# Kernel tuning notes

Hardware: AMD Instinct MI355X
Metric: run time of the kernel (lower is better)

## Reference

```python
import jax
import jax.numpy as jnp
import numpy as np

KSIZE, STRIDE, RATE, FUSE_K, SCALE = 3, 1, 2, 3, 10.0
ESCAPE_NAN = 1e-4


def _same_pad(x, k, s):
    # replicates torch same_padding: asymmetric zero pad so out = ceil(H/s)
    H, W = x.shape[2], x.shape[3]
    oh, ow = -(-H // s), -(-W // s)
    ph = max(0, (oh - 1) * s + k - H)
    pw = max(0, (ow - 1) * s + k - W)
    return jnp.pad(x, ((0, 0), (0, 0), (ph // 2, ph - ph // 2), (pw // 2, pw - pw // 2)))


def _extract_patches(x, k, s):
    # torch extract_image_patches: -> [B, L, C, k, k] with L = out_h*out_w
    x = _same_pad(x, k, s)
    B, C, H, W = x.shape
    Ho, Wo = (H - k) // s + 1, (W - k) // s + 1
    slices = [x[:, :, i:i + Ho * s:s, j:j + Wo * s:s] for i in range(k) for j in range(k)]
    p = jnp.stack(slices, axis=2).reshape(B, C, k, k, Ho, Wo)
    return p.transpose(0, 4, 5, 1, 2, 3).reshape(B, Ho * Wo, C, k, k)


def _contextual_attention(f, b, mask):
    dn = ('NCHW', 'OIHW', 'NCHW')
    # raw background patches for the final deconv: k = 2*rate, stride = rate
    raw_pat = _extract_patches(b, 2 * RATE, RATE * STRIDE)  # [B, L, C, 4, 4]
    # nearest-neighbor 1/rate downsample (torch F.interpolate nearest, sf=0.5)
    f_ds = f[:, :, ::RATE, ::RATE]
    b_ds = b[:, :, ::RATE, ::RATE]
    m_ds = mask[:, :, ::RATE, ::RATE]
    B, C, Hf, Wf = f_ds.shape
    Hb, Wb = b_ds.shape[2], b_ds.shape[3]
    b_pat = _extract_patches(b_ds, KSIZE, STRIDE)  # [B, L, C, 3, 3], L = Hb*Wb
    m_pat = _extract_patches(m_ds, KSIZE, STRIDE)[0]  # [L, 1, 3, 3] (first sample only, as in torch)
    mm = (jnp.mean(m_pat, axis=(1, 2, 3)) == 0.0).astype(f.dtype)[None, :, None, None]  # [1, L, 1, 1]
    fuse_w = jnp.eye(FUSE_K, dtype=f.dtype).reshape(1, 1, FUSE_K, FUSE_K)

    def per_item(xi, wi, raw_wi):
        # xi: [C,Hf,Wf]; wi: [L,C,3,3]; raw_wi: [L,C,4,4]
        max_wi = jnp.sqrt(jnp.sum(wi * wi + ESCAPE_NAN, axis=(1, 2, 3), keepdims=True))
        wi_n = wi / max_wi
        # matching conv: scores [1, L, Hf, Wf]
        yi = jax.lax.conv_general_dilated(xi[None], wi_n, (1, 1), ((1, 1), (1, 1)), dimension_numbers=dn)
        # fuse: identity-diagonal 3x3 conv along (bg_idx, fg_idx) twice with transposes
        yi = yi.reshape(1, 1, Hb * Wb, Hf * Wf)
        yi = jax.lax.conv_general_dilated(yi, fuse_w, (1, 1), ((1, 1), (1, 1)), dimension_numbers=dn)
        yi = yi.reshape(Hb, Wb, Hf, Wf).transpose(1, 0, 3, 2).reshape(1, 1, Hb * Wb, Hf * Wf)
        yi = jax.lax.conv_general_dilated(yi, fuse_w, (1, 1), ((1, 1), (1, 1)), dimension_numbers=dn)
        yi = yi.reshape(Wb, Hb, Wf, Hf).transpose(1, 0, 3, 2).reshape(1, Hb * Wb, Hf, Wf)
        yi = yi * mm
        yi = jax.nn.softmax(yi * SCALE, axis=1) * mm
        # conv_transpose2d(yi, raw_wi[I=L,O=C], stride=rate, padding=1) / 4
        w2 = jnp.flip(raw_wi, (2, 3)).transpose(1, 0, 2, 3)  # [C, L, 4, 4]
        pad = 2 * RATE - 1 - 1  # k - 1 - torch_padding = 2
        out = jax.lax.conv_general_dilated(yi, w2, (1, 1), ((pad, pad), (pad, pad)),
                                           lhs_dilation=(RATE, RATE), dimension_numbers=dn) / 4.0
        return out[0]

    return jax.vmap(per_item)(f_ds, b_pat, raw_pat)  # [B, C, H, W]


def setup_inputs() -> dict:
    key = jax.random.key(0)
    k1, k2 = jax.random.split(key)
    B, C, H, W = 2, 128, 128, 128
    f = jax.random.normal(k1, (B, C, H, W), dtype=jnp.float32)
    b = jax.random.normal(k2, (B, C, H, W), dtype=jnp.float32)
    mask = jnp.zeros((B, 1, H, W), dtype=jnp.float32)
    return {"f": f, "b": b, "mask": mask}


def reference(f, b, mask):
    return _contextual_attention(f, b, mask)
```

## Files before the change

### kernel.cpp

```cpp
#include <hip/hip_runtime.h>
#include <math.h>

#define CDIM 128
#define HF   128
#define WF   128
#define NP   4096
#define NCHUNK 64

typedef __attribute__((ext_vector_type(8))) short short8;
typedef float __attribute__((ext_vector_type(4), aligned(16))) f4a16;
typedef float __attribute__((ext_vector_type(4), aligned(4)))  f4u;

__device__ inline ushort f2bf(float x) {
  union { float f; unsigned u; } v; v.f = x;
  unsigned r = v.u + 0x7fff + ((v.u >> 16) & 1);
  return (ushort)(r >> 16);
}
__device__ inline float bf2f(ushort h) {
  union { unsigned u; float f; } v; v.u = ((unsigned)h) << 16; return v.f;
}

__device__ inline void gl2lds16(const ushort* g, ushort* l) {
  __builtin_amdgcn_global_load_lds((const __attribute__((address_space(1))) void*)g,
                                   (__attribute__((address_space(3))) void*)l, 16, 0, 0);
}

__global__ __launch_bounds__(256) void k_prep(const float* __restrict__ f,
                                              const float* __restrict__ b,
                                              ushort* __restrict__ fcat,
                                              ushort* __restrict__ bcat,
                                              float* __restrict__ s2) {
  int idx = blockIdx.x * 256 + threadIdx.x;
  int c = idx & 127, pos = idx >> 7;
  int x = pos & 63, y = pos >> 6;
  int src = c * 16384 + y * 256 + x * 2;
  float fv = f[src], bv = b[src];
  ushort fh = f2bf(fv); ushort fl = f2bf(fv - bf2f(fh));
  ushort bh = f2bf(bv); ushort bl = f2bf(bv - bf2f(bh));
  size_t base = (size_t)pos * 384;
  fcat[base + c] = fh; fcat[base + 128 + c] = fl; fcat[base + 256 + c] = fh;
  bcat[base + c] = bh; bcat[base + 128 + c] = bh; bcat[base + 256 + c] = bl;
  float sq = bv * bv;
#pragma unroll
  for (int off = 32; off; off >>= 1) sq += __shfl_down(sq, off);
  __shared__ float wsum[4];
  if ((threadIdx.x & 63) == 0) wsum[threadIdx.x >> 6] = sq;
  __syncthreads();
  if (threadIdx.x == 0) s2[blockIdx.x * 2]     = wsum[0] + wsum[1];
  if (threadIdx.x == 1) s2[blockIdx.x * 2 + 1] = wsum[2] + wsum[3];
}

__global__ __launch_bounds__(256) void k_mmpnorm(const float* __restrict__ mask,
                                                 const float* __restrict__ s2,
                                                 float* __restrict__ mmp,
                                                 float* __restrict__ rnrm) {
  int bx = blockIdx.x, t = threadIdx.x;
  if (bx < 16) {
    int a = bx * 256 + t;
    int yb = a & 63, xb = a >> 6;
    float s = 0.f;
    for (int dy = -1; dy <= 1; ++dy)
      for (int dx = -1; dx <= 1; ++dx) {
        int y = yb + dy, x = xb + dx;
        if ((unsigned)y < 64u && (unsigned)x < 64u)
          s += mask[y * 256 + x * 2];
      }
    mmp[a] = (s == 0.0f) ? 1.0f : 0.0f;
  } else {
    int p = (bx - 16) * 256 + t;
    int xb = p & 63, yb = p >> 6;
    float s = 0.f;
    for (int dy = -1; dy <= 1; ++dy)
      for (int dx = -1; dx <= 1; ++dx) {
        int y = yb + dy, x = xb + dx;
        if ((unsigned)y < 64u && (unsigned)x < 64u) s += s2[y * 64 + x];
      }
    rnrm[p] = rsqrtf(s + 1152.0f * 1.0e-4f);
  }
}

__global__ __launch_bounds__(256) void k_mfma_gemm(const ushort* __restrict__ A,
                                                   const ushort* __restrict__ B,
                                                   float* __restrict__ Out,
                                                   int Kdim, int lda, int ldb, int ldo,
                                                   size_t kz, size_t oz) {
  A += (size_t)blockIdx.z * kz; B += (size_t)blockIdx.z * kz;
  Out += (size_t)blockIdx.z * oz;
  __shared__ ushort As[128 * 64];
  __shared__ ushort Bs[128 * 64];
  int tid = threadIdx.x;
  int wave = tid >> 6, lane = tid & 63;
  int quad = lane >> 4, l16 = lane & 15;
  int m0 = blockIdx.y * 128, n0 = blockIdx.x * 128;
  int wm = (wave >> 1) * 64, wn = (wave & 1) * 64;
  int srow = lane >> 3;
  int g = lane & 7;
  int gperm = (g ^ srow) * 8;

  f4a16 acc[4][4];
#pragma unroll
  for (int i = 0; i < 4; ++i)
#pragma unroll
    for (int j = 0; j < 4; ++j) acc[i][j] = (f4a16){0.f, 0.f, 0.f, 0.f};

  for (int k0 = 0; k0 < Kdim; k0 += 64) {
#pragma unroll
    for (int i = 0; i < 4; ++i) {
      int rbase = wave * 32 + i * 8;
      gl2lds16(A + (size_t)(m0 + rbase + srow) * lda + k0 + gperm, &As[rbase * 64]);
      gl2lds16(B + (size_t)(n0 + rbase + srow) * ldb + k0 + gperm, &Bs[rbase * 64]);
    }
    __syncthreads();
#pragma unroll
    for (int s = 0; s < 2; ++s) {
      short8 afrag[4], bfrag[4];
#pragma unroll
      for (int t = 0; t < 4; ++t) {
        int am = wm + t * 16 + l16;
        int ga = ((s * 4 + quad) ^ (am & 7)) * 8;
        afrag[t] = *reinterpret_cast<const short8*>(&As[am * 64 + ga]);
        int bn = wn + t * 16 + l16;
        int gb = ((s * 4 + quad) ^ (bn & 7)) * 8;
        bfrag[t] = *reinterpret_cast<const short8*>(&Bs[bn * 64 + gb]);
      }
#pragma unroll
      for (int i = 0; i < 4; ++i)
#pragma unroll
        for (int j = 0; j < 4; ++j)
          acc[i][j] = __builtin_amdgcn_mfma_f32_16x16x32_bf16(afrag[i], bfrag[j], acc[i][j], 0, 0, 0);
    }
    __syncthreads();
  }
#pragma unroll
  for (int i = 0; i < 4; ++i)
#pragma unroll
    for (int j = 0; j < 4; ++j)
#pragma unroll
      for (int r = 0; r < 4; ++r)
        Out[(size_t)(m0 + wm + i * 16 + quad * 4 + r) * ldo + (n0 + wn + j * 16 + l16)] = acc[i][j][r];
}

__global__ __launch_bounds__(256) void k_s0(const float* __restrict__ D,
                                            const float* __restrict__ rnrm,
                                            float* __restrict__ S0) {
  int p = blockIdx.x;
  int yb = p >> 6, xb = p & 63;
  float rp = rnrm[p];
  int t = threadIdx.x;
#pragma unroll
  for (int it = 0; it < 4; ++it) {
    int q = (it * 256 + t) << 2;
    int qy = q >> 6, qx = q & 63;
    f4a16 acc = (f4a16){0.f, 0.f, 0.f, 0.f};
#pragma unroll
    for (int dy = -1; dy <= 1; ++dy) {
      if ((unsigned)(yb + dy) >= 64u) continue;
      if ((unsigned)(qy + dy) >= 64u) continue;
#pragma unroll
      for (int dx = -1; dx <= 1; ++dx) {
        if ((unsigned)(xb + dx) >= 64u) continue;
        int delta = dy * 64 + dx;
        const float* base = D + (size_t)(p + delta) * 4096;
        f4u v;
        if (dx == -1 && qx == 0) {
          f4u r = *(const f4u*)(base + q + delta + 1);
          v = (f4u){0.f, r.x, r.y, r.z};
        } else {
          v = *(const f4u*)(base + q + delta);
          if (dx == 1 && qx == 60) v.w = 0.f;
        }
        acc += v;
      }
    }
    acc *= rp;
    *(f4a16*)(S0 + ((size_t)p << 12) + q) = acc;
  }
}

__global__ __launch_bounds__(256) void k_fuse1(const float* __restrict__ S0,
                                               float* __restrict__ Yp) {
  __shared__ float row[4160];
  int i = blockIdx.x;
  int t = threadIdx.x;
  const float* r0 = S0 + (size_t)(i - 1) * 4096;
  const float* r1 = S0 + (size_t)i * 4096;
  const float* r2 = S0 + (size_t)(i + 1) * 4096;
  bool up = (i > 0), dn = (i < 4095);
#pragma unroll
  for (int jj = 0; jj < 4; ++jj) {
    int j = (jj * 256 + t) << 2;
    f4u s = *(const f4u*)(r1 + j);
    if (up) {
      f4u a;
      if (j == 0) { f4u r = *(const f4u*)r0; a = (f4u){0.f, r.x, r.y, r.z}; }
      else a = *(const f4u*)(r0 + j - 1);
      s += a;
    }
    if (dn) {
      f4u d = *(const f4u*)(r2 + j + 1);
      if (j == 4092) d.w = 0.f;
      s += d;
    }
    int base = j + (j >> 6);
    row[base + 0] = s.x; row[base + 1] = s.y; row[base + 2] = s.z; row[base + 3] = s.w;
  }
  __syncthreads();
  int a = ((i & 63) << 6) | (i >> 6);
  float* orow = Yp + ((size_t)a << 12);
#pragma unroll
  for (int bb = 0; bb < 16; ++bb) {
    int b = bb * 256 + t;
    int jT = ((b & 63) << 6) | (b >> 6);
    orow[b] = row[jT + (jT >> 6)];
  }
}

__global__ __launch_bounds__(256) void k_smax_part(const float* __restrict__ Yp,
                                                   const float* __restrict__ mmp,
                                                   float* __restrict__ pm,
                                                   float* __restrict__ ps) {
  int v = (blockIdx.x * 256 + threadIdx.x) << 2;
  int chunk = blockIdx.y;
  f4a16 m = (f4a16){-1e30f, -1e30f, -1e30f, -1e30f};
  f4a16 s = (f4a16){0.f, 0.f, 0.f, 0.f};
  int u0 = chunk * (4096 / NCHUNK);
  for (int u = u0; u < u0 + (4096 / NCHUNK); ++u) {
    const float* row = Yp + ((size_t)u << 12);
    f4u tv = *(const f4u*)(row + v);
    if (u > 0) {
      f4u a;
      if (v == 0) { f4u r = *(const f4u*)(row - 4096); a = (f4u){0.f, r.x, r.y, r.z}; }
      else a = *(const f4u*)(row - 4096 + v - 1);
      tv += a;
    }
    if (u < 4095) {
      f4u d = *(const f4u*)(row + 4096 + v + 1);
      if (v == 4092) d.w = 0.f;
      tv += d;
    }
    float g = 10.0f * mmp[u];
    f4u x = tv * g;
#pragma unroll
    for (int l = 0; l < 4; ++l) {
      float xl = x[l];
      if (xl > m[l]) { s[l] = s[l] * __expf(m[l] - xl) + 1.0f; m[l] = xl; }
      else           { s[l] += __expf(xl - m[l]); }
    }
  }
  *(f4a16*)(pm + chunk * NP + v) = m;
  *(f4a16*)(ps + chunk * NP + v) = s;
}

__global__ __launch_bounds__(256) void k_smax_red(const float* __restrict__ pm,
                                                  const float* __restrict__ ps,
                                                  float* __restrict__ mcol,
                                                  float* __restrict__ rscol) {
  int v = (blockIdx.x * 256 + threadIdx.x) << 2;
  f4a16 m = *(const f4a16*)(pm + v);
  f4a16 s = *(const f4a16*)(ps + v);
  for (int ch = 1; ch < NCHUNK; ++ch) {
    f4a16 m2 = *(const f4a16*)(pm + ch * NP + v);
    f4a16 s2 = *(const f4a16*)(ps + ch * NP + v);
#pragma unroll
    for (int l = 0; l < 4; ++l) {
      if (m2[l] > m[l]) { s[l] = s[l] * __expf(m[l] - m2[l]) + s2[l]; m[l] = m2[l]; }
      else              { s[l] += s2[l] * __expf(m2[l] - m[l]); }
    }
  }
  *(f4a16*)(mcol + v) = m;
  f4a16 r;
#pragma unroll
  for (int l = 0; l < 4; ++l) r[l] = 1.0f / s[l];
  *(f4a16*)(rscol + v) = r;
}

__global__ __launch_bounds__(256) void k_attnT(const float* __restrict__ Yp,
                                               const float* __restrict__ mcol,
                                               const float* __restrict__ rscol,
                                               const float* __restrict__ mmp,
                                               ushort* __restrict__ AT) {
  __shared__ float T[64][65];
  int a0 = blockIdx.x * 64, b0 = blockIdx.y * 64;
  int t = threadIdx.x;
  int i = t >> 4, j4 = (t & 15) << 2;
#pragma unroll
  for (int r = 0; r < 4; ++r) {
    int al = r * 16 + i;
    int a = a0 + al;
    const float* row = Yp + ((size_t)a << 12);
    int b = b0 + j4;
    f4u y = *(const f4u*)(row + b);
    if (a > 0) {
      f4u u_;
      if (b == 0) { f4u rr = *(const f4u*)(row - 4096); u_ = (f4u){0.f, rr.x, rr.y, rr.z}; }
      else u_ = *(const f4u*)(row - 4096 + b - 1);
      y += u_;
    }
    if (a < 4095) {
      f4u d = *(const f4u*)(row + 4096 + b + 1);
      if (b == 4092) d.w = 0.f;
      y += d;
    }
    float g = mmp[a];
    f4a16 mc = *(const f4a16*)(mcol + b);
    f4a16 rs = *(const f4a16*)(rscol + b);
    f4u x = y * (10.0f * g);
#pragma unroll
    for (int l = 0; l < 4; ++l)
      T[al][j4 + l] = g * __expf(x[l] - mc[l]) * rs[l];
  }
  __syncthreads();
  int by0 = b0 >> 6;
  int c2 = (t & 31) << 1;
  int blb = t >> 5;
#pragma unroll
  for (int r = 0; r < 8; ++r) {
    int bl = r * 8 + blb;
    int q = bl * 64 + by0;
    unsigned lo = (unsigned)f2bf(T[c2][bl]);
    unsigned hi = (unsigned)f2bf(T[c2 + 1][bl]);
    *(unsigned*)(AT + ((size_t)q << 12) + a0 + c2) = lo | (hi << 16);
  }
}

__global__ __launch_bounds__(256) void k_vtT(const float* __restrict__ b,
                                             ushort* __restrict__ VtT) {
  __shared__ float T[64][65];
  int k2 = blockIdx.x;
  int t = threadIdx.x;
  int c = k2 >> 4, dy = (k2 >> 2) & 3, dx = k2 & 3;
  int px = t & 63;
#pragma unroll
  for (int r = 0; r < 16; ++r) {
    int py = r * 4 + (t >> 6);
    int sy = 2 * py + dy - 1, sx = 2 * px + dx - 1;
    float v = 0.f;
    if ((unsigned)sy < (unsigned)HF && (unsigned)sx < (unsigned)WF)
      v = b[c * 16384 + sy * 128 + sx];
    T[py][px] = v;
  }
  __syncthreads();
  ushort* orow = VtT + (size_t)k2 * 4096;
#pragma unroll
  for (int r = 0; r < 16; ++r) {
    int a = r * 256 + t;
    orow[a] = f2bf(T[a & 63][a >> 6]);
  }
}

__global__ __launch_bounds__(256) void k_scatter(const float* __restrict__ M,
                                                 float* __restrict__ out) {
  const float* M1 = M + 8388608;
  int idx = blockIdx.x * 256 + threadIdx.x;
  int ox = idx & 127, oy = (idx >> 7) & 127, c = idx >> 14;
  int qy[2], dyv[2], qx[2], dxv[2];
  if (oy & 1) { qy[0] = (oy - 1) >> 1; dyv[0] = 2; qy[1] = (oy + 1) >> 1; dyv[1] = 0; }
  else        { qy[0] = (oy >> 1) - 1; dyv[0] = 3; qy[1] = oy >> 1;       dyv[1] = 1; }
  if (ox & 1) { qx[0] = (ox - 1) >> 1; dxv[0] = 2; qx[1] = (ox + 1) >> 1; dxv[1] = 0; }
  else        { qx[0] = (ox >> 1) - 1; dxv[0] = 3; qx[1] = ox >> 1;       dxv[1] = 1; }
  float s = 0.f;
#pragma unroll
  for (int i = 0; i < 2; ++i) {
    if ((unsigned)qy[i] >= 64u) continue;
#pragma unroll
    for (int j = 0; j < 2; ++j) {
      if ((unsigned)qx[j] >= 64u) continue;
      size_t off = (size_t)(c * 16 + dyv[i] * 4 + dxv[j]) * NP + qy[i] * 64 + qx[j];
      s += M[off] + M1[off];
    }
  }
  out[idx] = 0.25f * s;
}

extern "C" void kernel_launch(void* const* d_in, const int* in_sizes, int n_in,
                              void* d_out, int out_size, void* d_ws, size_t ws_size,
                              hipStream_t stream) {
  const float* f_all = (const float*)d_in[0];
  const float* b_all = (const float*)d_in[1];
  const float* m_all = (const float*)d_in[2];
  float* out = (float*)d_out;

  float* ws = (float*)d_ws;
  float* bufD = ws;
  float* bufS = ws + 16777216;
  ushort* fcat = (ushort*)bufS;
  ushort* bcat = (ushort*)(bufS + 786432);
  float* S0  = bufS;
  float* Yp  = bufD;
  ushort* AT  = (ushort*)bufS;
  ushort* VtT = (ushort*)(bufS + 8388608);
  float* Mbuf = bufD;
  float* smalls = ws + 2 * 16777216;
  float* s2    = smalls;
  float* rnrm  = s2 + 4096;
  float* mmp   = rnrm + 4096;
  float* pm    = mmp + 4096;
  float* ps    = pm + NCHUNK * NP;
  float* mcol  = ps + NCHUNK * NP;
  float* rscol = mcol + 4096;

  const size_t zsF = (size_t)CDIM * HF * WF;
  const size_t zsM = (size_t)HF * WF;

  for (int it = 0; it < 2; ++it) {
    const float* f = f_all + it * zsF;
    const float* b = b_all + it * zsF;
    const float* mk = m_all + it * zsM;
    float* o = out + it * zsF;

    k_prep<<<2048, 256, 0, stream>>>(f, b, fcat, bcat, s2);
    k_mmpnorm<<<32, 256, 0, stream>>>(mk, s2, mmp, rnrm);
    k_mfma_gemm<<<dim3(32, 32, 1), 256, 0, stream>>>(bcat, fcat, bufD, 384, 384, 384, NP, 0, 0);
    k_s0<<<4096, 256, 0, stream>>>(bufD, rnrm, S0);
    k_fuse1<<<4096, 256, 0, stream>>>(S0, Yp);
    k_smax_part<<<dim3(4, NCHUNK), 256, 0, stream>>>(Yp, mmp, pm, ps);
    k_smax_red<<<4, 256, 0, stream>>>(pm, ps, mcol, rscol);
    k_attnT<<<dim3(64, 64), 256, 0, stream>>>(Yp, mcol, rscol, mmp, AT);
    k_vtT<<<2048, 256, 0, stream>>>(b, VtT);
    k_mfma_gemm<<<dim3(32, 16, 2), 256, 0, stream>>>(VtT, AT, Mbuf, 2048, NP, NP, NP,
                                                     2048, 8388608);
    k_scatter<<<8192, 256, 0, stream>>>(Mbuf, o);
  }
}
```

Before: 752.4 us.

## Fuse softmax reduction, attention transpose and value transpose; drop split-K in output GEMM

Merges the softmax chunk reduction, the attention-transpose and the value-transpose kernels into one epilogue launch. Each attention block recomputes its 64 column stats from the partial max/sum buffers. The second GEMM now runs the full K=4096 in one pass with 512 blocks, replacing the split-K over two z-slices (1024 blocks), so the scatter reads one buffer instead of summing two. It also vectorises the fuse1 transposed store and the AT bf16 stores to 16 bytes. Fewer launches and less intermediate traffic are traded for redundant stat reductions and lower GEMM parallelism with a longer serial K loop.

```diff
diff --git a/kernel.cpp b/kernel.cpp
--- a/kernel.cpp
+++ b/kernel.cpp
@@ -82,10 +82,7 @@
 __global__ __launch_bounds__(256) void k_mfma_gemm(const ushort* __restrict__ A,
                                                    const ushort* __restrict__ B,
                                                    float* __restrict__ Out,
-                                                   int Kdim, int lda, int ldb, int ldo,
-                                                   size_t kz, size_t oz) {
-  A += (size_t)blockIdx.z * kz; B += (size_t)blockIdx.z * kz;
-  Out += (size_t)blockIdx.z * oz;
+                                                   int Kdim, int lda, int ldb, int ldo) {
   __shared__ ushort As[128 * 64];
   __shared__ ushort Bs[128 * 64];
   int tid = threadIdx.x;
@@ -208,10 +205,15 @@
   int a = ((i & 63) << 6) | (i >> 6);
   float* orow = Yp + ((size_t)a << 12);
 #pragma unroll
-  for (int bb = 0; bb < 16; ++bb) {
-    int b = bb * 256 + t;
-    int jT = ((b & 63) << 6) | (b >> 6);
-    orow[b] = row[jT + (jT >> 6)];
+  for (int bb = 0; bb < 4; ++bb) {
+    int b4 = (bb * 256 + t) << 2;
+    f4a16 o;
+#pragma unroll
+    for (int k = 0; k < 4; ++k) {
+      int jT = (((b4 + k) & 63) << 6) | ((b4 + k) >> 6);
+      o[k] = row[jT + (jT >> 6)];
+    }
+    *(f4a16*)(orow + b4) = o;
   }
 }
 
@@ -251,106 +253,106 @@
   *(f4a16*)(ps + chunk * NP + v) = s;
 }
 
-__global__ __launch_bounds__(256) void k_smax_red(const float* __restrict__ pm,
+__global__ __launch_bounds__(256) void k_epilogue(const float* __restrict__ Yp,
+                                                  const float* __restrict__ pm,
                                                   const float* __restrict__ ps,
-                                                  float* __restrict__ mcol,
-                                                  float* __restrict__ rscol) {
-  int v = (blockIdx.x * 256 + threadIdx.x) << 2;
-  f4a16 m = *(const f4a16*)(pm + v);
-  f4a16 s = *(const f4a16*)(ps + v);
-  for (int ch = 1; ch < NCHUNK; ++ch) {
-    f4a16 m2 = *(const f4a16*)(pm + ch * NP + v);
-    f4a16 s2 = *(const f4a16*)(ps + ch * NP + v);
-#pragma unroll
-    for (int l = 0; l < 4; ++l) {
-      if (m2[l] > m[l]) { s[l] = s[l] * __expf(m[l] - m2[l]) + s2[l]; m[l] = m2[l]; }
-      else              { s[l] += s2[l] * __expf(m2[l] - m[l]); }
-    }
-  }
-  *(f4a16*)(mcol + v) = m;
-  f4a16 r;
-#pragma unroll
-  for (int l = 0; l < 4; ++l) r[l] = 1.0f / s[l];
-  *(f4a16*)(rscol + v) = r;
-}
-
-__global__ __launch_bounds__(256) void k_attnT(const float* __restrict__ Yp,
-                                               const float* __restrict__ mcol,
-                                               const float* __restrict__ rscol,
-                                               const float* __restrict__ mmp,
-                                               ushort* __restrict__ AT) {
+                                                  const float* __restrict__ mmp,
+                                                  ushort* __restrict__ AT,
+                                                  const float* __restrict__ bimg,
+                                                  ushort* __restrict__ VtT) {
   __shared__ float T[64][65];
-  int a0 = blockIdx.x * 64, b0 = blockIdx.y * 64;
+  __shared__ float pmS[4][64];
+  __shared__ float psS[4][64];
+  __shared__ float mS[64];
+  __shared__ float rsS[64];
+  int gx = blockIdx.x;
   int t = threadIdx.x;
-  int i = t >> 4, j4 = (t & 15) << 2;
-#pragma unroll
-  for (int r = 0; r < 4; ++r) {
-    int al = r * 16 + i;
-    int a = a0 + al;
-    const float* row = Yp + ((size_t)a << 12);
-    int b = b0 + j4;
-    f4u y = *(const f4u*)(row + b);
-    if (a > 0) {
-      f4u u_;
-      if (b == 0) { f4u rr = *(const f4u*)(row - 4096); u_ = (f4u){0.f, rr.x, rr.y, rr.z}; }
-      else u_ = *(const f4u*)(row - 4096 + b - 1);
-      y += u_;
-    }
-    if (a < 4095) {
-      f4u d = *(const f4u*)(row + 4096 + b + 1);
-      if (b == 4092) d.w = 0.f;
-      y += d;
-    }
-    float g = mmp[a];
-    f4a16 mc = *(const f4a16*)(mcol + b);
-    f4a16 rs = *(const f4a16*)(rscol + b);
-    f4u x = y * (10.0f * g);
-#pragma unroll
-    for (int l = 0; l < 4; ++l)
-      T[al][j4 + l] = g * __expf(x[l] - mc[l]) * rs[l];
-  }
-  __syncthreads();
-  int by0 = b0 >> 6;
-  int c2 = (t & 31) << 1;
-  int blb = t >> 5;
-#pragma unroll
-  for (int r = 0; r < 8; ++r) {
-    int bl = r * 8 + blb;
-    int q = bl * 64 + by0;
-    unsigned lo = (unsigned)f2bf(T[c2][bl]);
-    unsigned hi = (unsigned)f2bf(T[c2 + 1][bl]);
-    *(unsigned*)(AT + ((size_t)q << 12) + a0 + c2) = lo | (hi << 16);
-  }
-}
-
-__global__ __launch_bounds__(256) void k_vtT(const float* __restrict__ b,
-                                             ushort* __restrict__ VtT) {
-  __shared__ float T[64][65];
-  int k2 = blockIdx.x;
-  int t = threadIdx.x;
-  int c = k2 >> 4, dy = (k2 >> 2) & 3, dx = k2 & 3;
-  int px = t & 63;
-#pragma unroll
-  for (int r = 0; r < 16; ++r) {
-    int py = r * 4 + (t >> 6);
-    int sy = 2 * py + dy - 1, sx = 2 * px + dx - 1;
-    float v = 0.f;
-    if ((unsigned)sy < (unsigned)HF && (unsigned)sx < (unsigned)WF)
-      v = b[c * 16384 + sy * 128 + sx];
-    T[py][px] = v;
-  }
-  __syncthreads();
-  ushort* orow = VtT + (size_t)k2 * 4096;
-#pragma unroll
-  for (int r = 0; r < 16; ++r) {
-    int a = r * 256 + t;
-    orow[a] = f2bf(T[a & 63][a >> 6]);
+  if (gx < 4096) {
+    int a0 = (gx & 63) * 64, b0 = (gx >> 6) * 64;
+    int j = t & 63, grp = t >> 6;
+    float m = -1e30f, s = 0.f;
+    for (int ch = grp * 16; ch < grp * 16 + 16; ++ch) {
+      float m2 = pm[ch * NP + b0 + j], s2 = ps[ch * NP + b0 + j];
+      if (m2 > m) { s = s * __expf(m - m2) + s2; m = m2; }
+      else        { s += s2 * __expf(m2 - m); }
+    }
+    pmS[grp][j] = m; psS[grp][j] = s;
+    __syncthreads();
+    if (grp == 0) {
+      for (int g2 = 1; g2 < 4; ++g2) {
+        float m2 = pmS[g2][j], s2 = psS[g2][j];
+        if (m2 > m) { s = s * __expf(m - m2) + s2; m = m2; }
+        else        { s += s2 * __expf(m2 - m); }
+      }
+      mS[j] = m; rsS[j] = 1.0f / s;
+    }
+    __syncthreads();
+    int i = t >> 4, j4 = (t & 15) << 2;
+    f4a16 mc = *(const f4a16*)&mS[j4];
+    f4a16 rs = *(const f4a16*)&rsS[j4];
+#pragma unroll
+    for (int r = 0; r < 4; ++r) {
+      int al = r * 16 + i;
+      int a = a0 + al;
+      const float* row = Yp + ((size_t)a << 12);
+      int b = b0 + j4;
+      f4u y = *(const f4u*)(row + b);
+      if (a > 0) {
+        f4u u_;
+        if (b == 0) { f4u rr = *(const f4u*)(row - 4096); u_ = (f4u){0.f, rr.x, rr.y, rr.z}; }
+        else u_ = *(const f4u*)(row - 4096 + b - 1);
+        y += u_;
+      }
+      if (a < 4095) {
+        f4u d = *(const f4u*)(row + 4096 + b + 1);
+        if (b == 4092) d.w = 0.f;
+        y += d;
+      }
+      float g = mmp[a];
+      f4u x = y * (10.0f * g);
+#pragma unroll
+      for (int l = 0; l < 4; ++l)
+        T[al][j4 + l] = g * __expf(x[l] - mc[l]) * rs[l];
+    }
+    __syncthreads();
+    int by0 = b0 >> 6;
+    int cgrp = (t & 7) * 8;
+#pragma unroll
+    for (int pass = 0; pass < 2; ++pass) {
+      int bl = pass * 32 + (t >> 3);
+      int q = bl * 64 + by0;
+      uint4 w;
+      w.x = (unsigned)f2bf(T[cgrp + 0][bl]) | ((unsigned)f2bf(T[cgrp + 1][bl]) << 16);
+      w.y = (unsigned)f2bf(T[cgrp + 2][bl]) | ((unsigned)f2bf(T[cgrp + 3][bl]) << 16);
+      w.z = (unsigned)f2bf(T[cgrp + 4][bl]) | ((unsigned)f2bf(T[cgrp + 5][bl]) << 16);
+      w.w = (unsigned)f2bf(T[cgrp + 6][bl]) | ((unsigned)f2bf(T[cgrp + 7][bl]) << 16);
+      *(uint4*)(AT + ((size_t)q << 12) + a0 + cgrp) = w;
+    }
+  } else {
+    int k2 = gx - 4096;
+    int c = k2 >> 4, dy = (k2 >> 2) & 3, dx = k2 & 3;
+    int px = t & 63;
+#pragma unroll
+    for (int r = 0; r < 16; ++r) {
+      int py = r * 4 + (t >> 6);
+      int sy = 2 * py + dy - 1, sx = 2 * px + dx - 1;
+      float v = 0.f;
+      if ((unsigned)sy < (unsigned)HF && (unsigned)sx < (unsigned)WF)
+        v = bimg[c * 16384 + sy * 128 + sx];
+      T[py][px] = v;
+    }
+    __syncthreads();
+    ushort* orow = VtT + (size_t)k2 * 4096;
+#pragma unroll
+    for (int r = 0; r < 16; ++r) {
+      int a = r * 256 + t;
+      orow[a] = f2bf(T[a & 63][a >> 6]);
+    }
   }
 }
 
 __global__ __launch_bounds__(256) void k_scatter(const float* __restrict__ M,
                                                  float* __restrict__ out) {
-  const float* M1 = M + 8388608;
   int idx = blockIdx.x * 256 + threadIdx.x;
   int ox = idx & 127, oy = (idx >> 7) & 127, c = idx >> 14;
   int qy[2], dyv[2], qx[2], dxv[2];
@@ -365,8 +367,8 @@
 #pragma unroll
     for (int j = 0; j < 2; ++j) {
       if ((unsigned)qx[j] >= 64u) continue;
-      size_t off = (size_t)(c * 16 + dyv[i] * 4 + dxv[j]) * NP + qy[i] * 64 + qx[j];
-      s += M[off] + M1[off];
+      int k = c * 16 + dyv[i] * 4 + dxv[j];
+      s += M[(size_t)k * NP + qy[i] * 64 + qx[j]];
     }
   }
   out[idx] = 0.25f * s;
@@ -396,8 +398,6 @@
   float* mmp   = rnrm + 4096;
   float* pm    = mmp + 4096;
   float* ps    = pm + NCHUNK * NP;
-  float* mcol  = ps + NCHUNK * NP;
-  float* rscol = mcol + 4096;
 
   const size_t zsF = (size_t)CDIM * HF * WF;
   const size_t zsM = (size_t)HF * WF;
@@ -410,15 +410,12 @@
 
     k_prep<<<2048, 256, 0, stream>>>(f, b, fcat, bcat, s2);
     k_mmpnorm<<<32, 256, 0, stream>>>(mk, s2, mmp, rnrm);
-    k_mfma_gemm<<<dim3(32, 32, 1), 256, 0, stream>>>(bcat, fcat, bufD, 384, 384, 384, NP, 0, 0);
+    k_mfma_gemm<<<dim3(32, 32), 256, 0, stream>>>(bcat, fcat, bufD, 384, 384, 384, NP);
     k_s0<<<4096, 256, 0, stream>>>(bufD, rnrm, S0);
     k_fuse1<<<4096, 256, 0, stream>>>(S0, Yp);
     k_smax_part<<<dim3(4, NCHUNK), 256, 0, stream>>>(Yp, mmp, pm, ps);
-    k_smax_red<<<4, 256, 0, stream>>>(pm, ps, mcol, rscol);
-    k_attnT<<<dim3(64, 64), 256, 0, stream>>>(Yp, mcol, rscol, mmp, AT);
-    k_vtT<<<2048, 256, 0, stream>>>(b, VtT);
-    k_mfma_gemm<<<dim3(32, 16, 2), 256, 0, stream>>>(VtT, AT, Mbuf, 2048, NP, NP, NP,
-                                                     2048, 8388608);
+    k_epilogue<<<6144, 256, 0, stream>>>(Yp, pm, ps, mmp, AT, b, VtT);
+    k_mfma_gemm<<<dim3(32, 16), 256, 0, stream>>>(VtT, AT, Mbuf, NP, NP, NP, NP);
     k_scatter<<<8192, 256, 0, stream>>>(Mbuf, o);
   }
 }
```

After: 678.2 us. -9.9%, faster.
